# Optimization experiments

Measured on AMD Instinct MI355X. Metric: run time of the kernel, lower is better.

The kernel has to match this reference:

```python
import jax, jax.numpy as jnp
import numpy as np

NEG_SLOPE = 0.2

def gat_layer(x, src, dst, W, a_src, a_dst, bias, heads, out_ch, concat):
    N = x.shape[0]
    h = (x @ W).reshape(N, heads, out_ch)                      # [N,H,C]
    alpha_s = jnp.sum(h * a_src, axis=-1)                      # [N,H]
    alpha_d = jnp.sum(h * a_dst, axis=-1)                      # [N,H]
    e = jax.nn.leaky_relu(alpha_s[src] + alpha_d[dst], NEG_SLOPE)  # [E,H]
    m = jax.ops.segment_max(e, dst, num_segments=N)            # segment softmax over incoming edges
    e = jnp.exp(e - m[dst])
    denom = jax.ops.segment_sum(e, dst, num_segments=N)
    alpha = e / denom[dst]                                     # [E,H]
    out = jax.ops.segment_sum(alpha[:, :, None] * h[src], dst, num_segments=N)  # [N,H,C]
    out = out.reshape(N, heads * out_ch) if concat else out.mean(axis=1)
    return out + bias

def _glorot(key, shape, fan):
    return jax.random.normal(key, shape, dtype=jnp.float32) * (1.0 / np.sqrt(fan))

def setup_inputs() -> dict:
    key = jax.random.key(0)
    ks = jax.random.split(key, 16)
    N, E, F_IN, H = 50000, 1600000, 128, 2
    x = jax.random.normal(ks[0], (N, F_IN), dtype=jnp.float32)
    edge_index = jax.random.randint(ks[1], (2, E), 0, N, dtype=jnp.int32)
    w1  = _glorot(ks[2], (F_IN, H * 32), F_IN)
    as1 = _glorot(ks[3], (H, 32), 32); ad1 = _glorot(ks[4], (H, 32), 32)
    b1  = jnp.zeros((H * 32,), jnp.float32)
    w2  = _glorot(ks[5], (H * 32, H * 64), H * 32)
    as2 = _glorot(ks[6], (H, 64), 64); ad2 = _glorot(ks[7], (H, 64), 64)
    b2  = jnp.zeros((H * 64,), jnp.float32)
    # layer 3: 128 -> 64, heads=1, concat=False
    w3  = _glorot(ks[8], (H * 64, 64), H * 64)
    as3 = _glorot(ks[9], (1, 64), 64); ad3 = _glorot(ks[10], (1, 64), 64)
    b3  = jnp.zeros((64,), jnp.float32)
    fcw = _glorot(ks[11], (64, 512), 64)
    fcb = jnp.zeros((512,), jnp.float32)
    return dict(x=x, edge_index=edge_index, w1=w1, as1=as1, ad1=ad1, b1=b1,
                w2=w2, as2=as2, ad2=ad2, b2=b2, w3=w3, as3=as3, ad3=ad3, b3=b3,
                fcw=fcw, fcb=fcb)

def reference(x, edge_index, w1, as1, ad1, b1, w2, as2, ad2, b2, w3, as3, ad3, b3, fcw, fcb):
    N = x.shape[0]
    # PyG GATConv default: add self-loops
    loops = jnp.arange(N, dtype=edge_index.dtype)
    src = jnp.concatenate([edge_index[0], loops])
    dst = jnp.concatenate([edge_index[1], loops])
    h = jax.nn.relu(gat_layer(x, src, dst, w1, as1, ad1, b1, heads=2, out_ch=32, concat=True))
    h = jax.nn.relu(gat_layer(h, src, dst, w2, as2, ad2, b2, heads=2, out_ch=64, concat=True))
    h = jax.nn.relu(gat_layer(h, src, dst, w3, as3, ad3, b3, heads=1, out_ch=64, concat=False))
    return jax.nn.relu(h @ fcw + fcb)
```

## Files before the change

kernel.cpp:

```cpp
#include <hip/hip_runtime.h>
#include <hip/hip_fp16.h>
#include <math.h>


typedef _Float16 h2_t __attribute__((ext_vector_type(2)));
typedef _Float16 f16x8 __attribute__((ext_vector_type(8)));
typedef float f32x4 __attribute__((ext_vector_type(4)));

__device__ __forceinline__ h2_t as_h2(unsigned int u) {
    union { unsigned int u; h2_t h; } x; x.u = u; return x.h;
}

__device__ __forceinline__ float fdot2(h2_t a, h2_t b, float c) {
#if __has_builtin(__builtin_amdgcn_fdot2)
    return __builtin_amdgcn_fdot2(a, b, c, false);
#else
    return c + (float)a[0] * (float)b[0] + (float)a[1] * (float)b[1];
#endif
}

__global__ void fused_pre_kernel(
        const float* __restrict__ x, __half* __restrict__ xh, int n4,
        const float* __restrict__ w1, const float* __restrict__ w2,
        const float* __restrict__ w3, const float* __restrict__ fcw,
        __half* __restrict__ o1, __half* __restrict__ o2,
        __half* __restrict__ o3, __half* __restrict__ o4T,
        const int* __restrict__ ei, int E, int N,
        int* __restrict__ cnt, int* __restrict__ rank,
        int XB, int WB) {
    const int b = blockIdx.x;
    if (b < XB) {
        int i = b * 256 + threadIdx.x;
        if (i < n4) {
            float4 v = ((const float4*)x)[i];
            __half2 a, c;
            a.x = (__half)v.x; a.y = (__half)v.y;
            c.x = (__half)v.z; c.y = (__half)v.w;
            ((__half2*)xh)[2 * i]     = a;
            ((__half2*)xh)[2 * i + 1] = c;
        }
    } else if (b < XB + WB) {
        int i = (b - XB) * 256 + threadIdx.x;
        if (i < 8192)       o1[i]         = (__half)w1[i];
        else if (i < 16384) o2[i - 8192]  = (__half)w2[i - 8192];
        else if (i < 24576) o3[i - 16384] = (__half)w3[i - 16384];
        else if (i < 57344) {
            int j = i - 24576;
            int k = j >> 9, c = j & 511;
            o4T[c * 64 + k] = (__half)fcw[j];
        }
    } else {
        const int base = XB + WB;
        const int Etot = E + N;
        const int T = (gridDim.x - base) * 256;
        int e = (b - base) * 256 + threadIdx.x;
#pragma unroll 4
        for (int u = 0; u < 4; ++u, e += T) {
            if (e < Etot) {
                int dst = (e < E) ? ei[E + e] : (e - E);
                rank[e] = atomicAdd(&cnt[dst], 1);
            }
        }
    }
}

#define SCAN_NB 256

__global__ __launch_bounds__(256) void scanA_kernel(const int* __restrict__ cnt,
                                                    int N, int* __restrict__ bsum) {
    __shared__ int red[256];
    const int chunk = (N + SCAN_NB - 1) / SCAN_NB;
    const int lo = blockIdx.x * chunk;
    const int len = min(N - lo, chunk);
    int s = 0;
    for (int i = threadIdx.x; i < len; i += 256) s += cnt[lo + i];
    red[threadIdx.x] = s;
    __syncthreads();
    for (int off = 128; off >= 1; off >>= 1) {
        if (threadIdx.x < off) red[threadIdx.x] += red[threadIdx.x + off];
        __syncthreads();
    }
    if (threadIdx.x == 0) bsum[blockIdx.x] = red[0];
}

__global__ __launch_bounds__(256) void scanB_kernel(int* __restrict__ bsum,
                                                    int* __restrict__ bbase) {
    __shared__ int s[256];
    int v = bsum[threadIdx.x];
    s[threadIdx.x] = v;
    __syncthreads();
    for (int off = 1; off < 256; off <<= 1) {
        int t = (threadIdx.x >= off) ? s[threadIdx.x - off] : 0;
        __syncthreads();
        s[threadIdx.x] += t;
        __syncthreads();
    }
    bbase[threadIdx.x] = s[threadIdx.x] - v;
}

__global__ __launch_bounds__(256) void scanC_kernel(const int* __restrict__ cnt,
                                                    int N, int Etot,
                                                    const int* __restrict__ bbase,
                                                    int* __restrict__ row_ptr) {
    __shared__ int s[256];
    const int chunk = (N + SCAN_NB - 1) / SCAN_NB;
    const int lo = blockIdx.x * chunk;
    const int len = min(N - lo, chunk);
    const int t = threadIdx.x;
    int v = (t < len) ? cnt[lo + t] : 0;
    s[t] = v;
    __syncthreads();
    for (int off = 1; off < 256; off <<= 1) {
        int u = (t >= off) ? s[t - off] : 0;
        __syncthreads();
        s[t] += u;
        __syncthreads();
    }
    if (t < len) row_ptr[lo + t] = bbase[blockIdx.x] + s[t] - v;
    if (blockIdx.x == 0 && t == 0) row_ptr[N] = Etot;
}

__global__ void scatter_kernel(const int* __restrict__ ei, int E, int N,
                               const int* __restrict__ row_ptr,
                               const int* __restrict__ rank,
                               int* __restrict__ csr_src) {
    const int Etot = E + N;
    const int T = gridDim.x * blockDim.x;
    int e = blockIdx.x * blockDim.x + threadIdx.x;
#pragma unroll 4
    for (int u = 0; u < 4; ++u, e += T) {
        if (e < Etot) {
            int src, dst;
            if (e < E) { src = ei[e]; dst = ei[E + e]; }
            else       { src = e - E; dst = e - E; }
            csr_src[row_ptr[dst] + rank[e]] = src;
        }
    }
}

template <int K, int CHUNK, int RB, int ALPHA>
__global__ __launch_bounds__(256) void gemm16_kernel(
        const __half* __restrict__ in,
        const __half* __restrict__ Wh,
        __half* __restrict__ out,
        const float* __restrict__ a_src,
        const float* __restrict__ a_dst,
        float* __restrict__ alpS,
        float* __restrict__ alpD,
        int N, int M) {
    constexpr int PL = CHUNK / 64;
    constexpr int K4 = K / 4;
    __shared__ uint2 wlds[K4 * CHUNK];
    const unsigned short* wsrc = (const unsigned short*)Wh;
    for (int idx = threadIdx.x; idx < K4 * CHUNK; idx += 256) {
        int k4 = idx / CHUNK, c = idx % CHUNK;
        const unsigned short* wp = wsrc + (size_t)(4 * k4) * M + c;
        uint2 v;
        v.x = (unsigned int)wp[0]     | ((unsigned int)wp[M] << 16);
        v.y = (unsigned int)wp[2 * M] | ((unsigned int)wp[3 * M] << 16);
        wlds[idx] = v;
    }
    __syncthreads();

    const int wid  = threadIdx.x >> 6;
    const int lane = threadIdx.x & 63;

    float aSv[PL], aDv[PL];
#pragma unroll
    for (int j = 0; j < PL; ++j) {
        aSv[j] = a_src[lane + 64 * j];
        aDv[j] = a_dst[lane + 64 * j];
    }

    const int groups = (N + RB - 1) / RB;
    for (int g = blockIdx.x * 4 + wid; g < groups; g += gridDim.x * 4) {
        const int n0 = g * RB;
        const bool full = (n0 + RB <= N);

        float acc[RB][PL];
#pragma unroll
        for (int r = 0; r < RB; ++r)
#pragma unroll
            for (int j = 0; j < PL; ++j) acc[r][j] = 0.0f;

        const uint2* xp = (const uint2*)(in + (size_t)n0 * K);

        if (full) {
            uint2 xv[RB], xn[RB];
#pragma unroll
            for (int r = 0; r < RB; ++r) xv[r] = xp[r * K4];
#pragma unroll 2
            for (int k4 = 0; k4 < K4; ++k4) {
                if (k4 + 1 < K4) {
#pragma unroll
                    for (int r = 0; r < RB; ++r)
                        xn[r] = xp[r * K4 + k4 + 1];
                }
#pragma unroll
                for (int j = 0; j < PL; ++j) {
                    uint2 wv = wlds[k4 * CHUNK + lane + 64 * j];
#pragma unroll
                    for (int r = 0; r < RB; ++r) {
                        acc[r][j] = fdot2(as_h2(xv[r].x), as_h2(wv.x), acc[r][j]);
                        acc[r][j] = fdot2(as_h2(xv[r].y), as_h2(wv.y), acc[r][j]);
                    }
                }
                if (k4 + 1 < K4) {
#pragma unroll
                    for (int r = 0; r < RB; ++r) xv[r] = xn[r];
                }
            }
        } else {
#pragma unroll 1
            for (int k4 = 0; k4 < K4; ++k4) {
#pragma unroll 1
                for (int r = 0; r < RB; ++r) {
                    if (n0 + r >= N) break;
                    uint2 xr = xp[(size_t)r * K4 + k4];
#pragma unroll
                    for (int j = 0; j < PL; ++j) {
                        uint2 wv = wlds[k4 * CHUNK + lane + 64 * j];
                        acc[r][j] = fdot2(as_h2(xr.x), as_h2(wv.x), acc[r][j]);
                        acc[r][j] = fdot2(as_h2(xr.y), as_h2(wv.y), acc[r][j]);
                    }
                }
            }
        }

#pragma unroll
        for (int r = 0; r < RB; ++r) {
            if (!full && n0 + r >= N) break;
            const int n = n0 + r;
#pragma unroll
            for (int j = 0; j < PL; ++j)
                out[(size_t)n * M + lane + 64 * j] = (__half)acc[r][j];

            float ps[PL], pd[PL];
#pragma unroll
            for (int j = 0; j < PL; ++j) { ps[j] = acc[r][j] * aSv[j]; pd[j] = acc[r][j] * aDv[j]; }
            const int m0 = (ALPHA == 1) ? 16 : 32;
            for (int mm = m0; mm >= 1; mm >>= 1) {
#pragma unroll
                for (int j = 0; j < PL; ++j) {
                    ps[j] += __shfl_xor(ps[j], mm, 64);
                    pd[j] += __shfl_xor(pd[j], mm, 64);
                }
            }
            if (ALPHA == 1) {
                if ((lane & 31) == 0) {
                    int idx = n * 2 + (lane >> 5);
                    alpS[idx] = ps[0]; alpD[idx] = pd[0];
                }
            } else if (ALPHA == 2) {
                if (lane == 0) {
#pragma unroll
                    for (int j = 0; j < PL; ++j) {
                        alpS[n * 2 + j] = ps[j]; alpD[n * 2 + j] = pd[j];
                    }
                }
            } else {
                if (lane == 0) { alpS[n] = ps[0]; alpD[n] = pd[0]; }
            }
        }
    }
}

__global__ __launch_bounds__(256) void fcmfma_kernel(
        const __half* __restrict__ in,
        const __half* __restrict__ WT,
        const float* __restrict__ bias,
        float* __restrict__ out,
        int N, int NT) {
    const int wid  = threadIdx.x >> 6;
    const int lane = threadIdx.x & 63;
    const int cb = blockIdx.y * 256 + wid * 64;
    const int r  = lane & 15;
    const int kg = lane >> 4;

    f16x8 bfrag[4][2];
#pragma unroll
    for (int t = 0; t < 4; ++t)
#pragma unroll
        for (int kf = 0; kf < 2; ++kf)
            bfrag[t][kf] = *(const f16x8*)(WT + (size_t)(cb + t * 16 + r) * 64 + kf * 32 + kg * 8);
    float bs[4];
#pragma unroll
    for (int t = 0; t < 4; ++t) bs[t] = bias[cb + t * 16 + r];

    const int rt0 = blockIdx.x * 5;
#pragma unroll 1
    for (int q = 0; q < 5; ++q) {
        const int rt = rt0 + q;
        if (rt >= NT) break;
        const int n0 = rt * 16;
        f16x8 a0 = *(const f16x8*)(in + (size_t)(n0 + r) * 64 + kg * 8);
        f16x8 a1 = *(const f16x8*)(in + (size_t)(n0 + r) * 64 + 32 + kg * 8);
#pragma unroll
        for (int t = 0; t < 4; ++t) {
            f32x4 acc = {0.0f, 0.0f, 0.0f, 0.0f};
            acc = __builtin_amdgcn_mfma_f32_16x16x32_f16(a0, bfrag[t][0], acc, 0, 0, 0);
            acc = __builtin_amdgcn_mfma_f32_16x16x32_f16(a1, bfrag[t][1], acc, 0, 0, 0);
#pragma unroll
            for (int i = 0; i < 4; ++i) {
                int grow = n0 + kg * 4 + i;
                if (grow < N)
                    out[(size_t)grow * 512 + cb + t * 16 + r] = fmaxf(acc[i] + bs[t], 0.0f);
            }
        }
    }
}

template <int H, int C>
__global__ __launch_bounds__(256) void aggregate_kernel(
        const __half* __restrict__ h,
        const float* __restrict__ alpha_s,
        const float* __restrict__ alpha_d,
        const int* __restrict__ row_ptr,
        const int* __restrict__ csr_src,
        const float* __restrict__ bias,
        __half* __restrict__ out, int N) {
    constexpr int M = H * C;
    __shared__ int   ss[4][64];
    __shared__ float sp[4][128];
    const int wid  = threadIdx.x >> 6;
    const int lane = threadIdx.x & 63;
    const int n = blockIdx.x * 4 + wid;
    if (n >= N) return;

    const int lo = row_ptr[n], hi = row_ptr[n + 1];
    const int myhead = (H == 2) ? (lane / C) : 0;

    float adv[H];
#pragma unroll
    for (int t = 0; t < H; ++t) adv[t] = alpha_d[n * H + t];

    float m[H], den[H], acc = 0.0f;
#pragma unroll
    for (int t = 0; t < H; ++t) { m[t] = -INFINITY; den[t] = 0.0f; }

    for (int e0 = lo; e0 < hi; e0 += 64) {
        const int idx = e0 + lane;
        const bool valid = idx < hi;
        const int src_l = csr_src[valid ? idx : hi - 1];

        float lg[H];
        if (H == 2) {
            float2 as = ((const float2*)alpha_s)[src_l];
            lg[0] = as.x + adv[0];
            lg[1] = as.y + adv[1];
        } else {
            lg[0] = alpha_s[src_l] + adv[0];
        }
#pragma unroll
        for (int t = 0; t < H; ++t) {
            float v = lg[t];
            v = v > 0.0f ? v : 0.2f * v;
            lg[t] = valid ? v : -INFINITY;
        }
        float cm[H];
#pragma unroll
        for (int t = 0; t < H; ++t) cm[t] = lg[t];
        for (int mm = 32; mm >= 1; mm >>= 1) {
#pragma unroll
            for (int t = 0; t < H; ++t)
                cm[t] = fmaxf(cm[t], __shfl_xor(cm[t], mm, 64));
        }
        float sc[H];
#pragma unroll
        for (int t = 0; t < H; ++t) {
            float mnew = fmaxf(m[t], cm[t]);
            sc[t] = __expf(m[t] - mnew);
            den[t] *= sc[t];
            m[t] = mnew;
        }
        acc *= (H == 1) ? sc[0] : (myhead == 0 ? sc[0] : sc[1]);

        float p[H], dsum[H];
#pragma unroll
        for (int t = 0; t < H; ++t) { p[t] = __expf(lg[t] - m[t]); dsum[t] = p[t]; }
        for (int mm = 32; mm >= 1; mm >>= 1) {
#pragma unroll
            for (int t = 0; t < H; ++t)
                dsum[t] += __shfl_xor(dsum[t], mm, 64);
        }
#pragma unroll
        for (int t = 0; t < H; ++t) den[t] += dsum[t];

        ss[wid][lane] = src_l;
        if (H == 2) ((float2*)sp[wid])[lane] = make_float2(p[0], p[1]);
        else        sp[wid][lane] = p[0];

        int nu = hi - e0; if (nu > 64) nu = 64;
        int u = 0;
#pragma unroll 1
        for (; u + 8 <= nu; u += 8) {
            int su[8];
#pragma unroll
            for (int t = 0; t < 8; ++t)
                su[t] = __builtin_amdgcn_readfirstlane(ss[wid][u + t]);
            float hv[8];
#pragma unroll
            for (int t = 0; t < 8; ++t)
                hv[t] = __half2float(h[(size_t)su[t] * M + lane]);
            if (H == 2) {
                const float2* pb = (const float2*)sp[wid];
#pragma unroll
                for (int t = 0; t < 8; ++t) {
                    float2 q = pb[u + t];
                    acc += (myhead == 0 ? q.x : q.y) * hv[t];
                }
            } else {
#pragma unroll
                for (int t = 0; t < 8; ++t)
                    acc += sp[wid][u + t] * hv[t];
            }
        }
#pragma unroll 1
        for (; u < nu; ++u) {
            int su = __builtin_amdgcn_readfirstlane(ss[wid][u]);
            float hv = __half2float(h[(size_t)su * M + lane]);
            if (H == 2) {
                float2 q = ((const float2*)sp[wid])[u];
                acc += (myhead == 0 ? q.x : q.y) * hv;
            } else {
                acc += sp[wid][u] * hv;
            }
        }
    }

    float dv = (H == 1) ? den[0] : (myhead == 0 ? den[0] : den[1]);
    float v = acc / dv + bias[lane];
    out[(size_t)n * M + lane] = (__half)fmaxf(v, 0.0f);
}

__global__ __launch_bounds__(256) void aggregate2_kernel(
        const __half* __restrict__ h,
        const float* __restrict__ alpha_s,
        const float* __restrict__ alpha_d,
        const int* __restrict__ row_ptr,
        const int* __restrict__ csr_src,
        const float* __restrict__ bias,
        __half* __restrict__ out, int N) {
    __shared__ int   ss[4][64];
    __shared__ float sp[4][64];
    const int wid  = threadIdx.x >> 6;
    const int lane = threadIdx.x & 63;
    const int gw   = blockIdx.x * 4 + wid;
    const int n    = gw >> 1;
    const int hd   = gw & 1;
    if (n >= N) return;

    const int lo = row_ptr[n], hi = row_ptr[n + 1];
    const float adv = alpha_d[n * 2 + hd];

    float m = -INFINITY, den = 0.0f, acc = 0.0f;

    for (int e0 = lo; e0 < hi; e0 += 64) {
        const int idx = e0 + lane;
        const bool valid = idx < hi;
        const int src_l = csr_src[valid ? idx : hi - 1];

        float lg = alpha_s[src_l * 2 + hd] + adv;
        lg = lg > 0.0f ? lg : 0.2f * lg;
        if (!valid) lg = -INFINITY;

        float cm = lg;
        for (int mm = 32; mm >= 1; mm >>= 1)
            cm = fmaxf(cm, __shfl_xor(cm, mm, 64));

        float mnew = fmaxf(m, cm);
        float sc = __expf(m - mnew);
        den *= sc; acc *= sc; m = mnew;

        float p = __expf(lg - m), ds = p;
        for (int mm = 32; mm >= 1; mm >>= 1)
            ds += __shfl_xor(ds, mm, 64);
        den += ds;

        ss[wid][lane] = src_l;
        sp[wid][lane] = p;

        int nu = hi - e0; if (nu > 64) nu = 64;
        int u = 0;
#pragma unroll 1
        for (; u + 8 <= nu; u += 8) {
            int su[8];
#pragma unroll
            for (int t = 0; t < 8; ++t)
                su[t] = __builtin_amdgcn_readfirstlane(ss[wid][u + t]);
            float hv[8];
#pragma unroll
            for (int t = 0; t < 8; ++t)
                hv[t] = __half2float(h[(size_t)su[t] * 128 + hd * 64 + lane]);
#pragma unroll
            for (int t = 0; t < 8; ++t)
                acc += sp[wid][u + t] * hv[t];
        }
#pragma unroll 1
        for (; u < nu; ++u) {
            int su = __builtin_amdgcn_readfirstlane(ss[wid][u]);
            acc += sp[wid][u] * __half2float(h[(size_t)su * 128 + hd * 64 + lane]);
        }
    }

    float v = acc / den + bias[hd * 64 + lane];
    out[(size_t)n * 128 + hd * 64 + lane] = (__half)fmaxf(v, 0.0f);
}


extern "C" void kernel_launch(void* const* d_in, const int* in_sizes, int n_in,
                              void* d_out, int out_size, void* d_ws, size_t ws_size,
                              hipStream_t stream) {
    const float* x   = (const float*)d_in[0];
    const int*   ei  = (const int*)  d_in[1];
    const float* w1  = (const float*)d_in[2];
    const float* as1 = (const float*)d_in[3];
    const float* ad1 = (const float*)d_in[4];
    const float* b1  = (const float*)d_in[5];
    const float* w2  = (const float*)d_in[6];
    const float* as2 = (const float*)d_in[7];
    const float* ad2 = (const float*)d_in[8];
    const float* b2  = (const float*)d_in[9];
    const float* w3  = (const float*)d_in[10];
    const float* as3 = (const float*)d_in[11];
    const float* ad3 = (const float*)d_in[12];
    const float* b3  = (const float*)d_in[13];
    const float* fcw = (const float*)d_in[14];
    const float* fcb = (const float*)d_in[15];
    float* out = (float*)d_out;

    const int N = in_sizes[0] / 128;
    const int E = in_sizes[1] / 2;
    const int Etot = E + N;

    char* p = (char*)d_ws;
    auto alloc = [&](size_t bytes) {
        char* r = p;
        p += (bytes + 255) & ~(size_t)255;
        return r;
    };
    int*    cnt     = (int*)   alloc((size_t)N * 4);
    int*    row_ptr = (int*)   alloc((size_t)(N + 1) * 4);
    int*    rank    = (int*)   alloc((size_t)Etot * 4);
    int*    csr_src = (int*)   alloc((size_t)Etot * 4);
    int*    bsum    = (int*)   alloc((size_t)SCAN_NB * 4);
    int*    bbase   = (int*)   alloc((size_t)SCAN_NB * 4);
    __half* x16     = (__half*)alloc((size_t)N * 128 * 2);
    __half* bufA    = (__half*)alloc((size_t)N * 128 * 2);
    __half* bufB    = (__half*)alloc((size_t)N * 128 * 2);
    __half* bufC    = (__half*)alloc((size_t)(N + 16) * 64 * 2);
    __half* wh1     = (__half*)alloc((size_t)8192 * 2);
    __half* wh2     = (__half*)alloc((size_t)8192 * 2);
    __half* wh3     = (__half*)alloc((size_t)8192 * 2);
    __half* fcwT    = (__half*)alloc((size_t)32768 * 2);
    float*  alpS    = (float*) alloc((size_t)N * 2 * 4);
    float*  alpD    = (float*) alloc((size_t)N * 2 * 4);
    (void)ws_size; (void)n_in; (void)out_size;

    hipMemsetAsync(cnt, 0, (size_t)N * 4, stream);
    const int n4 = N * 32;
    const int XB = (n4 + 255) / 256;
    const int WB = 224;
    const int CB = (Etot / 4 + 255) / 256 + 1;
    fused_pre_kernel<<<XB + WB + CB, 256, 0, stream>>>(
        x, x16, n4, w1, w2, w3, fcw, wh1, wh2, wh3, fcwT,
        ei, E, N, cnt, rank, XB, WB);
    scanA_kernel<<<SCAN_NB, 256, 0, stream>>>(cnt, N, bsum);
    scanB_kernel<<<1, 256, 0, stream>>>(bsum, bbase);
    scanC_kernel<<<SCAN_NB, 256, 0, stream>>>(cnt, N, Etot, bbase, row_ptr);
    scatter_kernel<<<CB, 256, 0, stream>>>(ei, E, N, row_ptr, rank, csr_src);

    int gb  = (N + 3) / 4;
    int gb2 = (2 * N + 3) / 4;
    const int GB16 = 2048;

    gemm16_kernel<128, 64, 8, 1><<<dim3(GB16, 1), 256, 0, stream>>>(
        x16, wh1, bufA, as1, ad1, alpS, alpD, N, 64);
    aggregate_kernel<2, 32><<<gb, 256, 0, stream>>>(bufA, alpS, alpD, row_ptr, csr_src, b1, bufB, N);

    gemm16_kernel<64, 128, 8, 2><<<dim3(GB16, 1), 256, 0, stream>>>(
        bufB, wh2, bufA, as2, ad2, alpS, alpD, N, 128);
    aggregate2_kernel<<<gb2, 256, 0, stream>>>(bufA, alpS, alpD, row_ptr, csr_src, b2, bufB, N);

    gemm16_kernel<128, 64, 8, 3><<<dim3(GB16, 1), 256, 0, stream>>>(
        bufB, wh3, bufA, as3, ad3, alpS, alpD, N, 64);
    aggregate_kernel<1, 64><<<gb, 256, 0, stream>>>(bufA, alpS, alpD, row_ptr, csr_src, b3, bufC, N);

    const int NT = (N + 15) / 16;
    const int GX = (NT + 4) / 5;
    fcmfma_kernel<<<dim3(GX, 2), 256, 0, stream>>>(
        bufC, fcwT, fcb, out, N, NT);
}
```

Measured before the change: 606.0 us.

## Overlap degree counting with layer-1 GEMM in a split-grid kernel

Moves the atomic in-degree counting and rank assignment out of the conversion kernel and into extra blocks of the first GEMM launch. Half the grid runs the GEMM and half runs the counting loop, so the atomic-bound count can overlap the compute-bound GEMM. The scan and scatter now run after the first GEMM. The trade-off is that the GEMM gets fewer blocks (1024 instead of 2048) and competes with the atomic traffic for the device.

Result: faster. 584.7 us (-3.5%).

```diff
diff --git a/kernel.cpp b/kernel.cpp
--- a/kernel.cpp
+++ b/kernel.cpp
@@ -19,15 +19,13 @@
 #endif
 }
 
-__global__ void fused_pre_kernel(
+__global__ void cvt_kernel(
         const float* __restrict__ x, __half* __restrict__ xh, int n4,
         const float* __restrict__ w1, const float* __restrict__ w2,
         const float* __restrict__ w3, const float* __restrict__ fcw,
         __half* __restrict__ o1, __half* __restrict__ o2,
         __half* __restrict__ o3, __half* __restrict__ o4T,
-        const int* __restrict__ ei, int E, int N,
-        int* __restrict__ cnt, int* __restrict__ rank,
-        int XB, int WB) {
+        int XB) {
     const int b = blockIdx.x;
     if (b < XB) {
         int i = b * 256 + threadIdx.x;
@@ -39,7 +37,7 @@
             ((__half2*)xh)[2 * i]     = a;
             ((__half2*)xh)[2 * i + 1] = c;
         }
-    } else if (b < XB + WB) {
+    } else {
         int i = (b - XB) * 256 + threadIdx.x;
         if (i < 8192)       o1[i]         = (__half)w1[i];
         else if (i < 16384) o2[i - 8192]  = (__half)w2[i - 8192];
@@ -48,18 +46,6 @@
             int j = i - 24576;
             int k = j >> 9, c = j & 511;
             o4T[c * 64 + k] = (__half)fcw[j];
-        }
-    } else {
-        const int base = XB + WB;
-        const int Etot = E + N;
-        const int T = (gridDim.x - base) * 256;
-        int e = (b - base) * 256 + threadIdx.x;
-#pragma unroll 4
-        for (int u = 0; u < 4; ++u, e += T) {
-            if (e < Etot) {
-                int dst = (e < E) ? ei[E + e] : (e - E);
-                rank[e] = atomicAdd(&cnt[dst], 1);
-            }
         }
     }
 }
@@ -138,7 +124,7 @@
     }
 }
 
-template <int K, int CHUNK, int RB, int ALPHA>
+template <int K, int CHUNK, int RB, int ALPHA, bool COUNT>
 __global__ __launch_bounds__(256) void gemm16_kernel(
         const __half* __restrict__ in,
         const __half* __restrict__ Wh,
@@ -147,10 +133,27 @@
         const float* __restrict__ a_dst,
         float* __restrict__ alpS,
         float* __restrict__ alpD,
-        int N, int M) {
+        int N, int M,
+        const int* __restrict__ ei, int E,
+        int* __restrict__ cnt, int* __restrict__ rank,
+        int GGEMM) {
     constexpr int PL = CHUNK / 64;
     constexpr int K4 = K / 4;
     __shared__ uint2 wlds[K4 * CHUNK];
+
+    if (COUNT && blockIdx.x >= GGEMM) {
+        const int Etot = E + N;
+        const int T = (gridDim.x - GGEMM) * 256;
+        int e = (blockIdx.x - GGEMM) * 256 + threadIdx.x;
+#pragma unroll 1
+        for (; e < Etot; e += T) {
+            int dst = (e < E) ? ei[E + e] : (e - E);
+            rank[e] = atomicAdd(&cnt[dst], 1);
+        }
+        return;
+    }
+    const int GSTRIDE = COUNT ? GGEMM : gridDim.x;
+
     const unsigned short* wsrc = (const unsigned short*)Wh;
     for (int idx = threadIdx.x; idx < K4 * CHUNK; idx += 256) {
         int k4 = idx / CHUNK, c = idx % CHUNK;
@@ -173,7 +176,7 @@
     }
 
     const int groups = (N + RB - 1) / RB;
-    for (int g = blockIdx.x * 4 + wid; g < groups; g += gridDim.x * 4) {
+    for (int g = blockIdx.x * 4 + wid; g < groups; g += GSTRIDE * 4) {
         const int n0 = g * RB;
         const bool full = (n0 + RB <= N);
 
@@ -561,29 +564,32 @@
     const int n4 = N * 32;
     const int XB = (n4 + 255) / 256;
     const int WB = 224;
-    const int CB = (Etot / 4 + 255) / 256 + 1;
-    fused_pre_kernel<<<XB + WB + CB, 256, 0, stream>>>(
-        x, x16, n4, w1, w2, w3, fcw, wh1, wh2, wh3, fcwT,
-        ei, E, N, cnt, rank, XB, WB);
+    cvt_kernel<<<XB + WB, 256, 0, stream>>>(
+        x, x16, n4, w1, w2, w3, fcw, wh1, wh2, wh3, fcwT, XB);
+
+    int gb  = (N + 3) / 4;
+    int gb2 = (2 * N + 3) / 4;
+    const int GB16 = 2048;
+    const int GG1  = 1024;
+    const int GC1  = 1024;
+
+    gemm16_kernel<128, 64, 8, 1, true><<<dim3(GG1 + GC1, 1), 256, 0, stream>>>(
+        x16, wh1, bufA, as1, ad1, alpS, alpD, N, 64, ei, E, cnt, rank, GG1);
+
     scanA_kernel<<<SCAN_NB, 256, 0, stream>>>(cnt, N, bsum);
     scanB_kernel<<<1, 256, 0, stream>>>(bsum, bbase);
     scanC_kernel<<<SCAN_NB, 256, 0, stream>>>(cnt, N, Etot, bbase, row_ptr);
+    const int CB = (Etot / 4 + 255) / 256 + 1;
     scatter_kernel<<<CB, 256, 0, stream>>>(ei, E, N, row_ptr, rank, csr_src);
 
-    int gb  = (N + 3) / 4;
-    int gb2 = (2 * N + 3) / 4;
-    const int GB16 = 2048;
-
-    gemm16_kernel<128, 64, 8, 1><<<dim3(GB16, 1), 256, 0, stream>>>(
-        x16, wh1, bufA, as1, ad1, alpS, alpD, N, 64);
     aggregate_kernel<2, 32><<<gb, 256, 0, stream>>>(bufA, alpS, alpD, row_ptr, csr_src, b1, bufB, N);
 
-    gemm16_kernel<64, 128, 8, 2><<<dim3(GB16, 1), 256, 0, stream>>>(
-        bufB, wh2, bufA, as2, ad2, alpS, alpD, N, 128);
+    gemm16_kernel<64, 128, 8, 2, false><<<dim3(GB16, 1), 256, 0, stream>>>(
+        bufB, wh2, bufA, as2, ad2, alpS, alpD, N, 128, nullptr, 0, nullptr, nullptr, GB16);
     aggregate2_kernel<<<gb2, 256, 0, stream>>>(bufA, alpS, alpD, row_ptr, csr_src, b2, bufB, N);
 
-    gemm16_kernel<128, 64, 8, 3><<<dim3(GB16, 1), 256, 0, stream>>>(
-        bufB, wh3, bufA, as3, ad3, alpS, alpD, N, 64);
+    gemm16_kernel<128, 64, 8, 3, false><<<dim3(GB16, 1), 256, 0, stream>>>(
+        bufB, wh3, bufA, as3, ad3, alpS, alpD, N, 64, nullptr, 0, nullptr, nullptr, GB16);
     aggregate_kernel<1, 64><<<gb, 256, 0, stream>>>(bufA, alpS, alpD, row_ptr, csr_src, b3, bufC, N);
 
     const int NT = (N + 15) / 16;
```

## Fuse layer-1 GEMM with x conversion and edge counting in one kernel

Applied to the files above, without the earlier changes.

Replaces the separate fp32-to-fp16 conversion of x and the layer-1 GEMM with one fused kernel. It reads fp32 x directly, converts it in registers, and keeps the w1 weights packed as fp16 in LDS. The kernel runs concurrently with the edge degree-counting atomics and the conversion of the other weights, as separate block ranges of the same launch. This removes one kernel launch and the write and re-read of an N×128 fp16 copy of x. In exchange, fp32 x is read directly, so each row costs twice the bytes, and the conversion work is repeated inside the GEMM loop.

Measured after the change: 602.6 us. About the same (-0.6%).

```diff
diff --git a/kernel.cpp b/kernel.cpp
--- a/kernel.cpp
+++ b/kernel.cpp
@@ -9,6 +9,12 @@
 
 __device__ __forceinline__ h2_t as_h2(unsigned int u) {
     union { unsigned int u; h2_t h; } x; x.u = u; return x.h;
+}
+
+__device__ __forceinline__ unsigned int pack2(float a, float b) {
+    union { h2_t h; unsigned int u; } x;
+    x.h[0] = (_Float16)a; x.h[1] = (_Float16)b;
+    return x.u;
 }
 
 __device__ __forceinline__ float fdot2(h2_t a, h2_t b, float c) {
@@ -19,46 +25,123 @@
 #endif
 }
 
-__global__ void fused_pre_kernel(
-        const float* __restrict__ x, __half* __restrict__ xh, int n4,
-        const float* __restrict__ w1, const float* __restrict__ w2,
-        const float* __restrict__ w3, const float* __restrict__ fcw,
-        __half* __restrict__ o1, __half* __restrict__ o2,
-        __half* __restrict__ o3, __half* __restrict__ o4T,
-        const int* __restrict__ ei, int E, int N,
+__global__ __launch_bounds__(256) void layer1_fused_kernel(
+        const float* __restrict__ x,
+        const float* __restrict__ w1,
+        __half* __restrict__ out,
+        const float* __restrict__ a_src,
+        const float* __restrict__ a_dst,
+        float* __restrict__ alpS,
+        float* __restrict__ alpD,
+        int N,
+        const int* __restrict__ ei, int E,
         int* __restrict__ cnt, int* __restrict__ rank,
-        int XB, int WB) {
-    const int b = blockIdx.x;
-    if (b < XB) {
-        int i = b * 256 + threadIdx.x;
-        if (i < n4) {
-            float4 v = ((const float4*)x)[i];
-            __half2 a, c;
-            a.x = (__half)v.x; a.y = (__half)v.y;
-            c.x = (__half)v.z; c.y = (__half)v.w;
-            ((__half2*)xh)[2 * i]     = a;
-            ((__half2*)xh)[2 * i + 1] = c;
-        }
-    } else if (b < XB + WB) {
-        int i = (b - XB) * 256 + threadIdx.x;
-        if (i < 8192)       o1[i]         = (__half)w1[i];
-        else if (i < 16384) o2[i - 8192]  = (__half)w2[i - 8192];
-        else if (i < 24576) o3[i - 16384] = (__half)w3[i - 16384];
-        else if (i < 57344) {
-            int j = i - 24576;
-            int k = j >> 9, c = j & 511;
-            o4T[c * 64 + k] = (__half)fcw[j];
-        }
-    } else {
-        const int base = XB + WB;
+        const float* __restrict__ w2, const float* __restrict__ w3,
+        const float* __restrict__ fcw,
+        __half* __restrict__ o2, __half* __restrict__ o3,
+        __half* __restrict__ o4T,
+        int CNTB, int GEMMB) {
+    __shared__ uint2 wlds[32 * 64];
+
+    if (blockIdx.x < CNTB) {
         const int Etot = E + N;
-        const int T = (gridDim.x - base) * 256;
-        int e = (b - base) * 256 + threadIdx.x;
+        const int T = CNTB * 256;
+        int e = blockIdx.x * 256 + threadIdx.x;
 #pragma unroll 4
         for (int u = 0; u < 4; ++u, e += T) {
             if (e < Etot) {
                 int dst = (e < E) ? ei[E + e] : (e - E);
                 rank[e] = atomicAdd(&cnt[dst], 1);
+            }
+        }
+        return;
+    }
+    if (blockIdx.x >= CNTB + GEMMB) {
+        int i = (blockIdx.x - CNTB - GEMMB) * 256 + threadIdx.x;
+        if (i < 8192)       o2[i]         = (__half)w2[i];
+        else if (i < 16384) o3[i - 8192]  = (__half)w3[i - 8192];
+        else if (i < 49152) {
+            int j = i - 16384;
+            int k = j >> 9, c = j & 511;
+            o4T[c * 64 + k] = (__half)fcw[j];
+        }
+        return;
+    }
+
+    const int bid = blockIdx.x - CNTB;
+    for (int idx = threadIdx.x; idx < 32 * 64; idx += 256) {
+        int k4 = idx >> 6, c = idx & 63;
+        const float* wp = w1 + (size_t)(4 * k4) * 64 + c;
+        uint2 v;
+        v.x = pack2(wp[0], wp[64]);
+        v.y = pack2(wp[128], wp[192]);
+        wlds[idx] = v;
+    }
+    __syncthreads();
+
+    const int wid  = threadIdx.x >> 6;
+    const int lane = threadIdx.x & 63;
+    const float aSv = a_src[lane];
+    const float aDv = a_dst[lane];
+
+    const int groups = (N + 7) / 8;
+    for (int g = bid * 4 + wid; g < groups; g += GEMMB * 4) {
+        const int n0 = g * 8;
+        const bool full = (n0 + 8 <= N);
+
+        float acc[8];
+#pragma unroll
+        for (int r = 0; r < 8; ++r) acc[r] = 0.0f;
+
+        const float4* xp = (const float4*)(x + (size_t)n0 * 128);
+
+        if (full) {
+#pragma unroll 2
+            for (int k4 = 0; k4 < 32; ++k4) {
+                float4 xr[8];
+#pragma unroll
+                for (int r = 0; r < 8; ++r) xr[r] = xp[r * 32 + k4];
+                uint2 wv = wlds[k4 * 64 + lane];
+#pragma unroll
+                for (int r = 0; r < 8; ++r) {
+                    h2_t lo, hi;
+                    lo[0] = (_Float16)xr[r].x; lo[1] = (_Float16)xr[r].y;
+                    hi[0] = (_Float16)xr[r].z; hi[1] = (_Float16)xr[r].w;
+                    acc[r] = fdot2(lo, as_h2(wv.x), acc[r]);
+                    acc[r] = fdot2(hi, as_h2(wv.y), acc[r]);
+                }
+            }
+        } else {
+#pragma unroll 1
+            for (int k4 = 0; k4 < 32; ++k4) {
+                uint2 wv = wlds[k4 * 64 + lane];
+#pragma unroll 1
+                for (int r = 0; r < 8; ++r) {
+                    if (n0 + r >= N) break;
+                    float4 xr = xp[r * 32 + k4];
+                    h2_t lo, hi;
+                    lo[0] = (_Float16)xr.x; lo[1] = (_Float16)xr.y;
+                    hi[0] = (_Float16)xr.z; hi[1] = (_Float16)xr.w;
+                    acc[r] = fdot2(lo, as_h2(wv.x), acc[r]);
+                    acc[r] = fdot2(hi, as_h2(wv.y), acc[r]);
+                }
+            }
+        }
+
+#pragma unroll
+        for (int r = 0; r < 8; ++r) {
+            if (!full && n0 + r >= N) break;
+            const int n = n0 + r;
+            out[(size_t)n * 64 + lane] = (__half)acc[r];
+
+            float ps = acc[r] * aSv, pd = acc[r] * aDv;
+            for (int mm = 16; mm >= 1; mm >>= 1) {
+                ps += __shfl_xor(ps, mm, 64);
+                pd += __shfl_xor(pd, mm, 64);
+            }
+            if ((lane & 31) == 0) {
+                int idx = n * 2 + (lane >> 5);
+                alpS[idx] = ps; alpD[idx] = pd;
             }
         }
     }
@@ -238,20 +321,14 @@
             float ps[PL], pd[PL];
 #pragma unroll
             for (int j = 0; j < PL; ++j) { ps[j] = acc[r][j] * aSv[j]; pd[j] = acc[r][j] * aDv[j]; }
-            const int m0 = (ALPHA == 1) ? 16 : 32;
-            for (int mm = m0; mm >= 1; mm >>= 1) {
+            for (int mm = 32; mm >= 1; mm >>= 1) {
 #pragma unroll
                 for (int j = 0; j < PL; ++j) {
                     ps[j] += __shfl_xor(ps[j], mm, 64);
                     pd[j] += __shfl_xor(pd[j], mm, 64);
                 }
             }
-            if (ALPHA == 1) {
-                if ((lane & 31) == 0) {
-                    int idx = n * 2 + (lane >> 5);
-                    alpS[idx] = ps[0]; alpD[idx] = pd[0];
-                }
-            } else if (ALPHA == 2) {
+            if (ALPHA == 2) {
                 if (lane == 0) {
 #pragma unroll
                     for (int j = 0; j < PL; ++j) {
@@ -545,11 +622,9 @@
     int*    csr_src = (int*)   alloc((size_t)Etot * 4);
     int*    bsum    = (int*)   alloc((size_t)SCAN_NB * 4);
     int*    bbase   = (int*)   alloc((size_t)SCAN_NB * 4);
-    __half* x16     = (__half*)alloc((size_t)N * 128 * 2);
     __half* bufA    = (__half*)alloc((size_t)N * 128 * 2);
     __half* bufB    = (__half*)alloc((size_t)N * 128 * 2);
     __half* bufC    = (__half*)alloc((size_t)(N + 16) * 64 * 2);
-    __half* wh1     = (__half*)alloc((size_t)8192 * 2);
     __half* wh2     = (__half*)alloc((size_t)8192 * 2);
     __half* wh3     = (__half*)alloc((size_t)8192 * 2);
     __half* fcwT    = (__half*)alloc((size_t)32768 * 2);
@@ -558,24 +633,25 @@
     (void)ws_size; (void)n_in; (void)out_size;
 
     hipMemsetAsync(cnt, 0, (size_t)N * 4, stream);
-    const int n4 = N * 32;
-    const int XB = (n4 + 255) / 256;
-    const int WB = 224;
-    const int CB = (Etot / 4 + 255) / 256 + 1;
-    fused_pre_kernel<<<XB + WB + CB, 256, 0, stream>>>(
-        x, x16, n4, w1, w2, w3, fcw, wh1, wh2, wh3, fcwT,
-        ei, E, N, cnt, rank, XB, WB);
+
+    const int CNTB  = (Etot / 4 + 255) / 256 + 1;
+    const int GEMMB = 1024;
+    const int WB    = 192;
+    layer1_fused_kernel<<<CNTB + GEMMB + WB, 256, 0, stream>>>(
+        x, w1, bufA, as1, ad1, alpS, alpD, N,
+        ei, E, cnt, rank, w2, w3, fcw, wh2, wh3, fcwT,
+        CNTB, GEMMB);
+
     scanA_kernel<<<SCAN_NB, 256, 0, stream>>>(cnt, N, bsum);
     scanB_kernel<<<1, 256, 0, stream>>>(bsum, bbase);
     scanC_kernel<<<SCAN_NB, 256, 0, stream>>>(cnt, N, Etot, bbase, row_ptr);
+    const int CB = (Etot / 4 + 255) / 256 + 1;
     scatter_kernel<<<CB, 256, 0, stream>>>(ei, E, N, row_ptr, rank, csr_src);
 
     int gb  = (N + 3) / 4;
     int gb2 = (2 * N + 3) / 4;
     const int GB16 = 2048;
 
-    gemm16_kernel<128, 64, 8, 1><<<dim3(GB16, 1), 256, 0, stream>>>(
-        x16, wh1, bufA, as1, ad1, alpS, alpD, N, 64);
     aggregate_kernel<2, 32><<<gb, 256, 0, stream>>>(bufA, alpS, alpD, row_ptr, csr_src, b1, bufB, N);
 
     gemm16_kernel<64, 128, 8, 2><<<dim3(GB16, 1), 256, 0, stream>>>(
```
